# Kernel optimization log

Hardware: AMD Instinct MI355X
Metric: run time of the kernel (lower is better)

The kernel has to match this reference:

```python
import jax, jax.numpy as jnp
import numpy as np

H, DK, DV, DM = 16, 64, 64, 1024
TEMP = float(np.power(DK, 0.5))
EPS = 1e-5


def setup_inputs() -> dict:
    key = jax.random.key(0)
    ks = jax.random.split(key, 12)
    B, LQ, LK = 2, 2048, 2048
    q = jax.random.normal(ks[0], (B, LQ, DM), jnp.float32)
    k = jax.random.normal(ks[1], (B, LK, DM), jnp.float32)
    v = jax.random.normal(ks[2], (B, LK, DM), jnp.float32)
    # projection weights, torch Linear convention: W [out, in], y = x @ W.T + b
    Wq = jax.random.normal(ks[3], (H * DK, DM), jnp.float32) * np.sqrt(2.0 / (DM + DK))
    Wk = jax.random.normal(ks[4], (H * DK, DM), jnp.float32) * np.sqrt(2.0 / (DM + DK))
    Wv = jax.random.normal(ks[5], (H * DV, DM), jnp.float32) * np.sqrt(2.0 / (DM + DV))
    bq = jnp.zeros((H * DK,), jnp.float32)
    bk = jnp.zeros((H * DK,), jnp.float32)
    bv = jnp.zeros((H * DV,), jnp.float32)
    Wfc = jax.random.normal(ks[6], (DM, H * DV), jnp.float32) * np.sqrt(2.0 / (DM + H * DV))
    bfc = jnp.zeros((DM,), jnp.float32)
    gamma = jnp.ones((DM,), jnp.float32)
    beta = jnp.zeros((DM,), jnp.float32)
    return {"q": q, "k": k, "v": v, "Wq": Wq, "bq": bq, "Wk": Wk, "bk": bk,
            "Wv": Wv, "bv": bv, "Wfc": Wfc, "bfc": bfc, "gamma": gamma, "beta": beta}


def reference(q, k, v, Wq, bq, Wk, bk, Wv, bv, Wfc, bfc, gamma, beta):
    B, LQ, _ = q.shape
    LK = k.shape[1]
    residual = q
    qh = (q @ Wq.T + bq).reshape(B, LQ, H, DK)   # [b, lq, h, dk]
    kh = (k @ Wk.T + bk).reshape(B, LK, H, DK)
    vh = (v @ Wv.T + bv).reshape(B, LK, H, DV)
    # scaled dot-product attention (scores laid out [h, b, lq, lk] to match (h*b) bmm)
    scores = jnp.einsum('bqhd,bkhd->hbqk', qh, kh) / TEMP
    attn = jax.nn.softmax(scores, axis=-1)
    ctx = jnp.einsum('hbqk,bkhd->bqhd', attn, vh).reshape(B, LQ, H * DV)
    out = ctx @ Wfc.T + bfc
    x = out + residual
    mean = jnp.mean(x, axis=-1, keepdims=True)
    var = jnp.var(x, axis=-1, keepdims=True)
    y = (x - mean) / jnp.sqrt(var + EPS) * gamma + beta
    attn_flat = attn.reshape(H * B, LQ, LK)
    q_flat = jnp.transpose(qh, (2, 0, 1, 3)).reshape(H * B, LQ, DK)
    return (y, attn_flat, q_flat)
```

## Files before the change

### kernel.cpp

```cpp
#include <hip/hip_runtime.h>

#define SCALE 0.125f

typedef __attribute__((ext_vector_type(8))) __bf16 bf16x8;
typedef __attribute__((ext_vector_type(4))) float f32x4;

__device__ __forceinline__ unsigned short f2bf(float f) {
    union { float f; unsigned u; } v; v.f = f;
    unsigned r = v.u + 0x7FFF + ((v.u >> 16) & 1);
    return (unsigned short)(r >> 16);
}
__device__ __forceinline__ unsigned pack2bf(float a, float b) {
    return (unsigned)f2bf(a) | ((unsigned)f2bf(b) << 16);
}
#define AS1(p) ((const __attribute__((address_space(1))) void*)(p))
#define AS3(p) ((__attribute__((address_space(3))) void*)(p))

__global__ __launch_bounds__(256) void convert_w_kernel(
    const float* __restrict__ Wq, const float* __restrict__ Wk,
    const float* __restrict__ Wv, const float* __restrict__ Wfc,
    unsigned short* __restrict__ wb)
{
    int t = blockIdx.x * 256 + threadIdx.x;
    int i = t * 8;
    int a = i >> 20;
    int off = i & 1048575;
    const float* src = a == 0 ? Wq : a == 1 ? Wk : a == 2 ? Wv : Wfc;
    float4 v0 = *(const float4*)(src + off);
    float4 v1 = *(const float4*)(src + off + 4);
    unsigned short u[8];
    u[0] = f2bf(v0.x); u[1] = f2bf(v0.y); u[2] = f2bf(v0.z); u[3] = f2bf(v0.w);
    u[4] = f2bf(v1.x); u[5] = f2bf(v1.y); u[6] = f2bf(v1.z); u[7] = f2bf(v1.w);
    *(int4*)&wb[i] = *(int4*)u;
}

__global__ __launch_bounds__(256) void qkv_proj_kernel(
    const float* __restrict__ q, const float* __restrict__ k, const float* __restrict__ v,
    const float* __restrict__ Wq, const float* __restrict__ Wk, const float* __restrict__ Wv,
    const float* __restrict__ bq, const float* __restrict__ bk, const float* __restrict__ bv,
    const unsigned short* __restrict__ Wb,
    unsigned short* __restrict__ qh, unsigned short* __restrict__ kh, unsigned short* __restrict__ vh,
    float* __restrict__ qflat)
{
    __shared__ unsigned short lds_a[128 * 40];
    __shared__ unsigned short lds_b[128 * 40];

    const int nb = blockIdx.x;
    const int mb = blockIdx.y;
    const int proj = nb >> 3;
    const int n0 = (nb & 7) * 128;
    const int m0 = mb * 128;

    const float* X    = proj == 0 ? q  : proj == 1 ? k  : v;
    const float* W    = proj == 0 ? Wq : proj == 1 ? Wk : Wv;
    const float* bias = proj == 0 ? bq : proj == 1 ? bk : bv;
    const unsigned short* WB = Wb ? Wb + (size_t)proj * 1048576 : (const unsigned short*)0;
    unsigned short* OUT = proj == 0 ? qh : proj == 1 ? kh : vh;

    const int t = threadIdx.x;
    const int l = t & 63;
    const int w = t >> 6;
    const int wr = w >> 1, wc = w & 1;
    const int li = l & 15, g = l >> 4;

    f32x4 acc[4][4];
    #pragma unroll
    for (int i = 0; i < 4; i++)
        #pragma unroll
        for (int j = 0; j < 4; j++) acc[i][j] = (f32x4){0.f, 0.f, 0.f, 0.f};

    for (int k0 = 0; k0 < 1024; k0 += 32) {
        #pragma unroll
        for (int i = 0; i < 4; i++) {
            int e = i * 1024 + t * 4;
            int r = e >> 5, c = e & 31;
            float4 av = *(const float4*)(X + (size_t)(m0 + r) * 1024 + k0 + c);
            ushort4 ua; ua.x = f2bf(av.x); ua.y = f2bf(av.y); ua.z = f2bf(av.z); ua.w = f2bf(av.w);
            *(ushort4*)&lds_a[r * 40 + c] = ua;
        }
        if (WB) {
            #pragma unroll
            for (int i = 0; i < 2; i++) {
                int e8 = i * 256 + t;
                int r = e8 >> 2, c8 = e8 & 3;
                int4 wv = *(const int4*)(WB + (size_t)(n0 + r) * 1024 + k0 + c8 * 8);
                *(int4*)&lds_b[r * 40 + c8 * 8] = wv;
            }
        } else {
            #pragma unroll
            for (int i = 0; i < 4; i++) {
                int e = i * 1024 + t * 4;
                int r = e >> 5, c = e & 31;
                float4 bw = *(const float4*)(W + (size_t)(n0 + r) * 1024 + k0 + c);
                ushort4 ub; ub.x = f2bf(bw.x); ub.y = f2bf(bw.y); ub.z = f2bf(bw.z); ub.w = f2bf(bw.w);
                *(ushort4*)&lds_b[r * 40 + c] = ub;
            }
        }
        __syncthreads();
        bf16x8 af[4], bfr[4];
        #pragma unroll
        for (int mi = 0; mi < 4; mi++)
            af[mi] = *(bf16x8*)&lds_a[(wr * 64 + mi * 16 + li) * 40 + g * 8];
        #pragma unroll
        for (int ni = 0; ni < 4; ni++)
            bfr[ni] = *(bf16x8*)&lds_b[(wc * 64 + ni * 16 + li) * 40 + g * 8];
        #pragma unroll
        for (int mi = 0; mi < 4; mi++)
            #pragma unroll
            for (int ni = 0; ni < 4; ni++)
                acc[mi][ni] = __builtin_amdgcn_mfma_f32_16x16x32_bf16(af[mi], bfr[ni], acc[mi][ni], 0, 0, 0);
        __syncthreads();
    }

    #pragma unroll
    for (int mi = 0; mi < 4; mi++)
        #pragma unroll
        for (int ni = 0; ni < 4; ni++) {
            int col = n0 + wc * 64 + ni * 16 + li;
            float bl = bias[col];
            #pragma unroll
            for (int j = 0; j < 4; j++) {
                int row = m0 + wr * 64 + mi * 16 + g * 4 + j;
                float val = acc[mi][ni][j] + bl;
                OUT[(size_t)row * 1024 + col] = f2bf(val);
                if (proj == 0) {
                    int hh = col >> 6, dk = col & 63;
                    int bb = row >> 11, lq = row & 2047;
                    __builtin_nontemporal_store(val,
                        qflat + (((size_t)(hh * 2 + bb)) * 2048 + lq) * 64 + dk);
                }
            }
        }
}

__global__ __launch_bounds__(512) void attn_kernel(
    const unsigned short* __restrict__ qh, const unsigned short* __restrict__ kh,
    const unsigned short* __restrict__ vh, float* __restrict__ attn_out,
    unsigned short* __restrict__ ctx)
{
    __shared__ unsigned short lds_kv[64 * 136];
    __shared__ unsigned short lds_p[128 * 128];

    const int qt = blockIdx.x, hb = blockIdx.y;
    const int h = hb >> 1, b_ = hb & 1;
    const int q0 = qt * 128;
    const int t = threadIdx.x, l = t & 63, w = t >> 6;
    const int li = l & 15, g = l >> 4;

    const unsigned short* Qb = qh + (size_t)(b_ * 2048 + q0) * 1024 + h * 64;
    const unsigned short* Kb = kh + (size_t)(b_ * 2048) * 1024 + h * 64;
    const unsigned short* Vb = vh + (size_t)(b_ * 2048) * 1024 + h * 64;
    float* Ab = attn_out + ((size_t)hb * 2048 + q0) * 2048;

    bf16x8 aq[2];
    #pragma unroll
    for (int kk = 0; kk < 2; kk++)
        aq[kk] = *(const bf16x8*)(Qb + (size_t)(w * 16 + li) * 1024 + kk * 32 + g * 8);

#define STAGE_K(KT) do { \
    _Pragma("unroll") \
    for (int c = 0; c < 2; c++) { \
        int r_ = w * 16 + c * 8 + (l >> 3); \
        int c16s = (l & 7) ^ (r_ & 7); \
        const unsigned short* gp = Kb + (size_t)((KT) * 128 + r_) * 1024 + c16s * 8; \
        __builtin_amdgcn_global_load_lds(AS1(gp), AS3(lds_kv + w * 1024 + c * 512), 16, 0, 0); \
    } } while (0)

    float ssum = 0.f;
    for (int kt = 0; kt < 16; kt++) {
        __syncthreads();
        STAGE_K(kt);
        __syncthreads();
        f32x4 s[8];
        #pragma unroll
        for (int ni = 0; ni < 8; ni++) s[ni] = (f32x4){0.f, 0.f, 0.f, 0.f};
        #pragma unroll
        for (int kk = 0; kk < 2; kk++)
            #pragma unroll
            for (int ni = 0; ni < 8; ni++) {
                int row = ni * 16 + li;
                int us_ = (4 * kk + g) ^ (li & 7);
                bf16x8 bk = *(bf16x8*)&lds_kv[row * 64 + us_ * 8];
                s[ni] = __builtin_amdgcn_mfma_f32_16x16x32_bf16(bk, aq[kk], s[ni], 0, 0, 0);
            }
        float ps = 0.f;
        #pragma unroll
        for (int ni = 0; ni < 8; ni++)
            #pragma unroll
            for (int j = 0; j < 4; j++) ps += __expf(s[ni][j] * SCALE);
        ssum += ps;
    }
    ssum += __shfl_xor(ssum, 16, 64);
    ssum += __shfl_xor(ssum, 32, 64);
    const float rl = 1.f / ssum;

    f32x4 cacc[4];
    #pragma unroll
    for (int ni = 0; ni < 4; ni++) cacc[ni] = (f32x4){0.f, 0.f, 0.f, 0.f};

    for (int kt = 0; kt < 16; kt++) {
        __syncthreads();
        STAGE_K(kt);
        __syncthreads();
        f32x4 s[8];
        #pragma unroll
        for (int ni = 0; ni < 8; ni++) s[ni] = (f32x4){0.f, 0.f, 0.f, 0.f};
        #pragma unroll
        for (int kk = 0; kk < 2; kk++)
            #pragma unroll
            for (int ni = 0; ni < 8; ni++) {
                int row = ni * 16 + li;
                int us_ = (4 * kk + g) ^ (li & 7);
                bf16x8 bk = *(bf16x8*)&lds_kv[row * 64 + us_ * 8];
                s[ni] = __builtin_amdgcn_mfma_f32_16x16x32_bf16(bk, aq[kk], s[ni], 0, 0, 0);
            }
        __syncthreads();
        #pragma unroll
        for (int i = 0; i < 2; i++) {
            int e8 = i * 512 + t;
            int lk = e8 >> 3;
            int dg = (e8 & 7) * 8;
            int4 val = *(const int4*)(Vb + (size_t)(kt * 128 + lk) * 1024 + dg);
            unsigned short us[8]; *(int4*)us = val;
            #pragma unroll
            for (int ii = 0; ii < 8; ii++) {
                int d = dg + ii;
                int lks = lk ^ (((d >> 3) & 7) << 3);
                lds_kv[d * 136 + lks] = us[ii];
            }
        }
        #pragma unroll
        for (int ni = 0; ni < 8; ni++) {
            float p0 = __expf(s[ni][0] * SCALE) * rl;
            float p1 = __expf(s[ni][1] * SCALE) * rl;
            float p2 = __expf(s[ni][2] * SCALE) * rl;
            float p3 = __expf(s[ni][3] * SCALE) * rl;
            f32x4 pv4 = (f32x4){p0, p1, p2, p3};
            __builtin_nontemporal_store(pv4,
                (f32x4*)(Ab + (size_t)(w * 16 + li) * 2048 + kt * 128 + ni * 16 + 4 * g));
            int u = 2 * ni + (g >> 1);
            int us_ = u ^ (li & 7);
            int base = (w * 16 + li) * 128 + us_ * 8 + 4 * (g & 1);
            *(unsigned*)&lds_p[base]     = pack2bf(p0, p1);
            *(unsigned*)&lds_p[base + 2] = pack2bf(p2, p3);
        }
        __syncthreads();
        #pragma unroll
        for (int ks = 0; ks < 4; ks++) {
            int up = (4 * ks + g) ^ (li & 7);
            bf16x8 ap = *(bf16x8*)&lds_p[(w * 16 + li) * 128 + up * 8];
            #pragma unroll
            for (int ni = 0; ni < 4; ni++) {
                int d = ni * 16 + li;
                int lkb = (ks * 32 + g * 8) ^ (((d >> 3) & 7) << 3);
                bf16x8 bv2 = *(bf16x8*)&lds_kv[d * 136 + lkb];
                cacc[ni] = __builtin_amdgcn_mfma_f32_16x16x32_bf16(ap, bv2, cacc[ni], 0, 0, 0);
            }
        }
    }
#undef STAGE_K

    #pragma unroll
    for (int ni = 0; ni < 4; ni++)
        #pragma unroll
        for (int j = 0; j < 4; j++) {
            int r = w * 16 + g * 4 + j;
            int d = ni * 16 + li;
            ctx[(size_t)(b_ * 2048 + q0 + r) * 1024 + h * 64 + d] = f2bf(cacc[ni][j]);
        }
}

__global__ __launch_bounds__(256) void fc_kernel(
    const unsigned short* __restrict__ ctx, const float* __restrict__ Wfc,
    const unsigned short* __restrict__ Wfcb,
    const float* __restrict__ bfc, const float* __restrict__ resid,
    float* __restrict__ xout)
{
    __shared__ unsigned short lds_a[128 * 40];
    __shared__ unsigned short lds_b[128 * 40];

    const int n0 = blockIdx.x * 128;
    const int m0 = blockIdx.y * 128;
    const int t = threadIdx.x, l = t & 63, w = t >> 6;
    const int wr = w >> 1, wc = w & 1;
    const int li = l & 15, g = l >> 4;

    f32x4 acc[4][4];
    #pragma unroll
    for (int i = 0; i < 4; i++)
        #pragma unroll
        for (int j = 0; j < 4; j++) acc[i][j] = (f32x4){0.f, 0.f, 0.f, 0.f};

    for (int k0 = 0; k0 < 1024; k0 += 32) {
        #pragma unroll
        for (int i = 0; i < 2; i++) {
            int e = i * 2048 + t * 8;
            int r = e >> 5, c = e & 31;
            int4 val = *(const int4*)(ctx + (size_t)(m0 + r) * 1024 + k0 + c);
            *(int4*)&lds_a[r * 40 + c] = val;
        }
        if (Wfcb) {
            #pragma unroll
            for (int i = 0; i < 2; i++) {
                int e8 = i * 256 + t;
                int r = e8 >> 2, c8 = e8 & 3;
                int4 wv = *(const int4*)(Wfcb + (size_t)(n0 + r) * 1024 + k0 + c8 * 8);
                *(int4*)&lds_b[r * 40 + c8 * 8] = wv;
            }
        } else {
            #pragma unroll
            for (int i = 0; i < 4; i++) {
                int e = i * 1024 + t * 4;
                int r = e >> 5, c = e & 31;
                float4 bw = *(const float4*)(Wfc + (size_t)(n0 + r) * 1024 + k0 + c);
                ushort4 ub; ub.x = f2bf(bw.x); ub.y = f2bf(bw.y); ub.z = f2bf(bw.z); ub.w = f2bf(bw.w);
                *(ushort4*)&lds_b[r * 40 + c] = ub;
            }
        }
        __syncthreads();
        bf16x8 af[4], bfr[4];
        #pragma unroll
        for (int mi = 0; mi < 4; mi++)
            af[mi] = *(bf16x8*)&lds_a[(wr * 64 + mi * 16 + li) * 40 + g * 8];
        #pragma unroll
        for (int ni = 0; ni < 4; ni++)
            bfr[ni] = *(bf16x8*)&lds_b[(wc * 64 + ni * 16 + li) * 40 + g * 8];
        #pragma unroll
        for (int mi = 0; mi < 4; mi++)
            #pragma unroll
            for (int ni = 0; ni < 4; ni++)
                acc[mi][ni] = __builtin_amdgcn_mfma_f32_16x16x32_bf16(af[mi], bfr[ni], acc[mi][ni], 0, 0, 0);
        __syncthreads();
    }

    #pragma unroll
    for (int mi = 0; mi < 4; mi++)
        #pragma unroll
        for (int ni = 0; ni < 4; ni++) {
            int col = n0 + wc * 64 + ni * 16 + li;
            float bl = bfc[col];
            #pragma unroll
            for (int j = 0; j < 4; j++) {
                int row = m0 + wr * 64 + mi * 16 + g * 4 + j;
                float val = acc[mi][ni][j] + bl + resid[(size_t)row * 1024 + col];
                xout[(size_t)row * 1024 + col] = val;
            }
        }
}

__global__ __launch_bounds__(256) void ln_kernel(
    const float* __restrict__ x, const float* __restrict__ gamma,
    const float* __restrict__ beta, float* __restrict__ y)
{
    __shared__ float red[2][4];
    const int row = blockIdx.x;
    const int t = threadIdx.x;
    float4 v = *(const float4*)(x + (size_t)row * 1024 + t * 4);
    float s = v.x + v.y + v.z + v.w;
    float ss = v.x * v.x + v.y * v.y + v.z * v.z + v.w * v.w;
    #pragma unroll
    for (int msk = 1; msk < 64; msk <<= 1) {
        s += __shfl_xor(s, msk, 64);
        ss += __shfl_xor(ss, msk, 64);
    }
    int w = t >> 6, l = t & 63;
    if (l == 0) { red[0][w] = s; red[1][w] = ss; }
    __syncthreads();
    s = red[0][0] + red[0][1] + red[0][2] + red[0][3];
    ss = red[1][0] + red[1][1] + red[1][2] + red[1][3];
    float mean = s * (1.f / 1024.f);
    float var = ss * (1.f / 1024.f) - mean * mean;
    float rstd = rsqrtf(var + 1e-5f);
    float4 g4 = *(const float4*)(gamma + t * 4);
    float4 b4 = *(const float4*)(beta + t * 4);
    float4 o;
    o.x = (v.x - mean) * rstd * g4.x + b4.x;
    o.y = (v.y - mean) * rstd * g4.y + b4.y;
    o.z = (v.z - mean) * rstd * g4.z + b4.z;
    o.w = (v.w - mean) * rstd * g4.w + b4.w;
    *(float4*)(y + (size_t)row * 1024 + t * 4) = o;
}

extern "C" void kernel_launch(void* const* d_in, const int* in_sizes, int n_in,
                              void* d_out, int out_size, void* d_ws, size_t ws_size,
                              hipStream_t stream)
{
    const float* q     = (const float*)d_in[0];
    const float* k     = (const float*)d_in[1];
    const float* v     = (const float*)d_in[2];
    const float* Wq    = (const float*)d_in[3];
    const float* bq    = (const float*)d_in[4];
    const float* Wk    = (const float*)d_in[5];
    const float* bk    = (const float*)d_in[6];
    const float* Wv    = (const float*)d_in[7];
    const float* bv    = (const float*)d_in[8];
    const float* Wfc   = (const float*)d_in[9];
    const float* bfc   = (const float*)d_in[10];
    const float* gamma = (const float*)d_in[11];
    const float* beta  = (const float*)d_in[12];

    float* y     = (float*)d_out;
    float* attn  = (float*)d_out + 4194304;
    float* qflat = (float*)d_out + 4194304 + 134217728;

    char* ws = (char*)d_ws;
    unsigned short* qh  = (unsigned short*)(ws);
    unsigned short* kh  = (unsigned short*)(ws + 8388608ull);
    unsigned short* vh  = (unsigned short*)(ws + 16777216ull);
    unsigned short* ctx = (unsigned short*)(ws + 25165824ull);
    float* x            = (float*)(ws + 33554432ull);
    unsigned short* Wb  = (unsigned short*)(ws + 50331648ull);
    const bool pre = ws_size >= 58720256ull;
    const unsigned short* Wbp = pre ? Wb : (const unsigned short*)0;

    if (pre)
        convert_w_kernel<<<2048, 256, 0, stream>>>(Wq, Wk, Wv, Wfc, Wb);
    qkv_proj_kernel<<<dim3(24, 32), 256, 0, stream>>>(q, k, v, Wq, Wk, Wv, bq, bk, bv,
                                                      Wbp, qh, kh, vh, qflat);
    attn_kernel<<<dim3(16, 32), 512, 0, stream>>>(qh, kh, vh, attn, ctx);
    fc_kernel<<<dim3(8, 32), 256, 0, stream>>>(ctx, Wfc, pre ? Wb + 3145728 : (const unsigned short*)0,
                                               bfc, q, x);
    ln_kernel<<<4096, 256, 0, stream>>>(x, gamma, beta, y);
}
```

Baseline: 318.9 us.

## Pre-convert activations to bf16, async LDS loads, double-buffer K and pre-transpose V

Activations q/k/v are converted to bf16 up front, staged temporarily in the attn output buffer. The QKV and FC GEMMs now use direct global-to-LDS loads with a 64-wide K step and swizzled layout. Attention double-buffers K tiles and reads V from a pre-transposed layout written by the QKV epilogue, which removes the scalar transpose scatter into LDS. LayerNorm runs in place on the output, and the workspace layout and launch bounds change. These changes add an extra conversion pass over the inputs and make correctness depend on the attn buffer being overwritten after use.

Result: faster. 309.9 us (-2.8%).

```diff
diff --git a/kernel.cpp b/kernel.cpp
--- a/kernel.cpp
+++ b/kernel.cpp
@@ -16,34 +16,44 @@
 #define AS1(p) ((const __attribute__((address_space(1))) void*)(p))
 #define AS3(p) ((__attribute__((address_space(3))) void*)(p))
 
-__global__ __launch_bounds__(256) void convert_w_kernel(
+__global__ __launch_bounds__(256) void convert_kernel(
+    const float* __restrict__ q, const float* __restrict__ k, const float* __restrict__ v,
     const float* __restrict__ Wq, const float* __restrict__ Wk,
     const float* __restrict__ Wv, const float* __restrict__ Wfc,
-    unsigned short* __restrict__ wb)
-{
-    int t = blockIdx.x * 256 + threadIdx.x;
-    int i = t * 8;
-    int a = i >> 20;
-    int off = i & 1048575;
-    const float* src = a == 0 ? Wq : a == 1 ? Wk : a == 2 ? Wv : Wfc;
+    unsigned short* __restrict__ xb, unsigned short* __restrict__ wb)
+{
+    size_t i = ((size_t)blockIdx.x * 256 + threadIdx.x) * 8;
+    const float* src;
+    unsigned short* dst;
+    size_t off;
+    if (i < 12582912ull) {
+        int a = (int)(i >> 22);
+        src = a == 0 ? q : a == 1 ? k : v;
+        off = i & 4194303ull;
+        dst = xb + i;
+    } else {
+        size_t wi = i - 12582912ull;
+        int a = (int)(wi >> 20);
+        src = a == 0 ? Wq : a == 1 ? Wk : a == 2 ? Wv : Wfc;
+        off = wi & 1048575ull;
+        dst = wb + wi;
+    }
     float4 v0 = *(const float4*)(src + off);
     float4 v1 = *(const float4*)(src + off + 4);
     unsigned short u[8];
     u[0] = f2bf(v0.x); u[1] = f2bf(v0.y); u[2] = f2bf(v0.z); u[3] = f2bf(v0.w);
     u[4] = f2bf(v1.x); u[5] = f2bf(v1.y); u[6] = f2bf(v1.z); u[7] = f2bf(v1.w);
-    *(int4*)&wb[i] = *(int4*)u;
-}
-
-__global__ __launch_bounds__(256) void qkv_proj_kernel(
-    const float* __restrict__ q, const float* __restrict__ k, const float* __restrict__ v,
-    const float* __restrict__ Wq, const float* __restrict__ Wk, const float* __restrict__ Wv,
+    *(int4*)dst = *(int4*)u;
+}
+
+__global__ __launch_bounds__(256, 3) void qkv_proj_kernel(
+    const unsigned short* __restrict__ xb, const unsigned short* __restrict__ wb,
     const float* __restrict__ bq, const float* __restrict__ bk, const float* __restrict__ bv,
-    const unsigned short* __restrict__ Wb,
-    unsigned short* __restrict__ qh, unsigned short* __restrict__ kh, unsigned short* __restrict__ vh,
-    float* __restrict__ qflat)
-{
-    __shared__ unsigned short lds_a[128 * 40];
-    __shared__ unsigned short lds_b[128 * 40];
+    unsigned short* __restrict__ qh, unsigned short* __restrict__ kh,
+    unsigned short* __restrict__ vht, float* __restrict__ qflat)
+{
+    __shared__ unsigned short lds_a[128 * 64];
+    __shared__ unsigned short lds_b[128 * 64];
 
     const int nb = blockIdx.x;
     const int mb = blockIdx.y;
@@ -51,17 +61,15 @@
     const int n0 = (nb & 7) * 128;
     const int m0 = mb * 128;
 
-    const float* X    = proj == 0 ? q  : proj == 1 ? k  : v;
-    const float* W    = proj == 0 ? Wq : proj == 1 ? Wk : Wv;
+    const unsigned short* A = xb + (size_t)proj * 4194304;
+    const unsigned short* B = wb + (size_t)proj * 1048576;
     const float* bias = proj == 0 ? bq : proj == 1 ? bk : bv;
-    const unsigned short* WB = Wb ? Wb + (size_t)proj * 1048576 : (const unsigned short*)0;
-    unsigned short* OUT = proj == 0 ? qh : proj == 1 ? kh : vh;
-
-    const int t = threadIdx.x;
-    const int l = t & 63;
-    const int w = t >> 6;
+
+    const int t = threadIdx.x, l = t & 63, w = t >> 6;
     const int wr = w >> 1, wc = w & 1;
     const int li = l & 15, g = l >> 4;
+    const int sr = l >> 3;
+    const int us_st = (l & 7) ^ sr;
 
     f32x4 acc[4][4];
     #pragma unroll
@@ -69,76 +77,84 @@
         #pragma unroll
         for (int j = 0; j < 4; j++) acc[i][j] = (f32x4){0.f, 0.f, 0.f, 0.f};
 
-    for (int k0 = 0; k0 < 1024; k0 += 32) {
+    for (int k0 = 0; k0 < 1024; k0 += 64) {
+        __syncthreads();
         #pragma unroll
         for (int i = 0; i < 4; i++) {
-            int e = i * 1024 + t * 4;
-            int r = e >> 5, c = e & 31;
-            float4 av = *(const float4*)(X + (size_t)(m0 + r) * 1024 + k0 + c);
-            ushort4 ua; ua.x = f2bf(av.x); ua.y = f2bf(av.y); ua.z = f2bf(av.z); ua.w = f2bf(av.w);
-            *(ushort4*)&lds_a[r * 40 + c] = ua;
-        }
-        if (WB) {
-            #pragma unroll
-            for (int i = 0; i < 2; i++) {
-                int e8 = i * 256 + t;
-                int r = e8 >> 2, c8 = e8 & 3;
-                int4 wv = *(const int4*)(WB + (size_t)(n0 + r) * 1024 + k0 + c8 * 8);
-                *(int4*)&lds_b[r * 40 + c8 * 8] = wv;
-            }
-        } else {
-            #pragma unroll
-            for (int i = 0; i < 4; i++) {
-                int e = i * 1024 + t * 4;
-                int r = e >> 5, c = e & 31;
-                float4 bw = *(const float4*)(W + (size_t)(n0 + r) * 1024 + k0 + c);
-                ushort4 ub; ub.x = f2bf(bw.x); ub.y = f2bf(bw.y); ub.z = f2bf(bw.z); ub.w = f2bf(bw.w);
-                *(ushort4*)&lds_b[r * 40 + c] = ub;
-            }
-        }
-        __syncthreads();
-        bf16x8 af[4], bfr[4];
+            int r = i * 32 + w * 8 + sr;
+            __builtin_amdgcn_global_load_lds(AS1(A + (size_t)(m0 + r) * 1024 + k0 + us_st * 8),
+                                             AS3(lds_a + (i * 256 + w * 64) * 8), 16, 0, 0);
+            __builtin_amdgcn_global_load_lds(AS1(B + (size_t)(n0 + r) * 1024 + k0 + us_st * 8),
+                                             AS3(lds_b + (i * 256 + w * 64) * 8), 16, 0, 0);
+        }
+        __syncthreads();
+        #pragma unroll
+        for (int kk = 0; kk < 2; kk++) {
+            bf16x8 af[4], bfr[4];
+            int us = (kk * 4 + g) ^ (li & 7);
+            #pragma unroll
+            for (int mi = 0; mi < 4; mi++)
+                af[mi] = *(bf16x8*)&lds_a[(wr * 64 + mi * 16 + li) * 64 + us * 8];
+            #pragma unroll
+            for (int ni = 0; ni < 4; ni++)
+                bfr[ni] = *(bf16x8*)&lds_b[(wc * 64 + ni * 16 + li) * 64 + us * 8];
+            #pragma unroll
+            for (int mi = 0; mi < 4; mi++)
+                #pragma unroll
+                for (int ni = 0; ni < 4; ni++)
+                    acc[mi][ni] = __builtin_amdgcn_mfma_f32_16x16x32_bf16(af[mi], bfr[ni], acc[mi][ni], 0, 0, 0);
+        }
+    }
+
+    if (proj == 2) {
         #pragma unroll
         for (int mi = 0; mi < 4; mi++)
-            af[mi] = *(bf16x8*)&lds_a[(wr * 64 + mi * 16 + li) * 40 + g * 8];
-        #pragma unroll
-        for (int ni = 0; ni < 4; ni++)
-            bfr[ni] = *(bf16x8*)&lds_b[(wc * 64 + ni * 16 + li) * 40 + g * 8];
+            #pragma unroll
+            for (int ni = 0; ni < 4; ni++) {
+                int c = n0 + wc * 64 + ni * 16 + li;
+                float bl = bias[c];
+                int hh = c >> 6, dd = c & 63;
+                int row0 = m0 + wr * 64 + mi * 16 + g * 4;
+                int bb = row0 >> 11, kk2 = row0 & 2047;
+                ushort4 u4;
+                u4.x = f2bf(acc[mi][ni][0] + bl);
+                u4.y = f2bf(acc[mi][ni][1] + bl);
+                u4.z = f2bf(acc[mi][ni][2] + bl);
+                u4.w = f2bf(acc[mi][ni][3] + bl);
+                *(ushort4*)(vht + ((size_t)((bb * 16 + hh) * 64 + dd)) * 2048 + kk2) = u4;
+            }
+    } else {
+        unsigned short* OUT = proj == 0 ? qh : kh;
         #pragma unroll
         for (int mi = 0; mi < 4; mi++)
             #pragma unroll
-            for (int ni = 0; ni < 4; ni++)
-                acc[mi][ni] = __builtin_amdgcn_mfma_f32_16x16x32_bf16(af[mi], bfr[ni], acc[mi][ni], 0, 0, 0);
-        __syncthreads();
-    }
-
-    #pragma unroll
-    for (int mi = 0; mi < 4; mi++)
-        #pragma unroll
-        for (int ni = 0; ni < 4; ni++) {
-            int col = n0 + wc * 64 + ni * 16 + li;
-            float bl = bias[col];
-            #pragma unroll
-            for (int j = 0; j < 4; j++) {
-                int row = m0 + wr * 64 + mi * 16 + g * 4 + j;
-                float val = acc[mi][ni][j] + bl;
-                OUT[(size_t)row * 1024 + col] = f2bf(val);
-                if (proj == 0) {
-                    int hh = col >> 6, dk = col & 63;
-                    int bb = row >> 11, lq = row & 2047;
-                    __builtin_nontemporal_store(val,
-                        qflat + (((size_t)(hh * 2 + bb)) * 2048 + lq) * 64 + dk);
+            for (int ni = 0; ni < 4; ni++) {
+                int c = n0 + wc * 64 + ni * 16 + li;
+                float bl = bias[c];
+                int hh = c >> 6, dd = c & 63;
+                int row0 = m0 + wr * 64 + mi * 16 + g * 4;
+                #pragma unroll
+                for (int j = 0; j < 4; j++) {
+                    int row = row0 + j;
+                    float val = acc[mi][ni][j] + bl;
+                    OUT[(size_t)row * 1024 + c] = f2bf(val);
+                    if (proj == 0) {
+                        int bb = row >> 11, lq = row & 2047;
+                        __builtin_nontemporal_store(val,
+                            qflat + (((size_t)(hh * 2 + bb)) * 2048 + lq) * 64 + dd);
+                    }
                 }
             }
-        }
-}
-
-__global__ __launch_bounds__(512) void attn_kernel(
+    }
+}
+
+__global__ __launch_bounds__(512, 4) void attn_kernel(
     const unsigned short* __restrict__ qh, const unsigned short* __restrict__ kh,
-    const unsigned short* __restrict__ vh, float* __restrict__ attn_out,
+    const unsigned short* __restrict__ vht, float* __restrict__ attn_out,
     unsigned short* __restrict__ ctx)
 {
-    __shared__ unsigned short lds_kv[64 * 136];
+    __shared__ unsigned short lds_k[2][128 * 64];
+    __shared__ unsigned short lds_vt[64 * 128];
     __shared__ unsigned short lds_p[128 * 128];
 
     const int qt = blockIdx.x, hb = blockIdx.y;
@@ -149,7 +165,7 @@
 
     const unsigned short* Qb = qh + (size_t)(b_ * 2048 + q0) * 1024 + h * 64;
     const unsigned short* Kb = kh + (size_t)(b_ * 2048) * 1024 + h * 64;
-    const unsigned short* Vb = vh + (size_t)(b_ * 2048) * 1024 + h * 64;
+    const unsigned short* VTb = vht + (size_t)(b_ * 16 + h) * 131072;
     float* Ab = attn_out + ((size_t)hb * 2048 + q0) * 2048;
 
     bf16x8 aq[2];
@@ -157,38 +173,48 @@
     for (int kk = 0; kk < 2; kk++)
         aq[kk] = *(const bf16x8*)(Qb + (size_t)(w * 16 + li) * 1024 + kk * 32 + g * 8);
 
-#define STAGE_K(KT) do { \
+    const int sr8 = l >> 3;
+    const int us8 = (l & 7) ^ sr8;
+
+#define STAGE_K(KT, BUF) do { \
     _Pragma("unroll") \
     for (int c = 0; c < 2; c++) { \
-        int r_ = w * 16 + c * 8 + (l >> 3); \
-        int c16s = (l & 7) ^ (r_ & 7); \
-        const unsigned short* gp = Kb + (size_t)((KT) * 128 + r_) * 1024 + c16s * 8; \
-        __builtin_amdgcn_global_load_lds(AS1(gp), AS3(lds_kv + w * 1024 + c * 512), 16, 0, 0); \
+        int r_ = w * 16 + c * 8 + sr8; \
+        __builtin_amdgcn_global_load_lds(AS1(Kb + (size_t)((KT) * 128 + r_) * 1024 + us8 * 8), \
+            AS3(lds_k[BUF] + w * 1024 + c * 512), 16, 0, 0); \
     } } while (0)
 
+    const int vd0 = w * 4 + g;
+    const int vd1 = vd0 + 32;
+    const int vslot0 = (li ^ (vd0 & 7)) * 8;
+    const int vslot1 = (li ^ (vd1 & 7)) * 8;
+
     float ssum = 0.f;
+    int cur = 0;
+    STAGE_K(0, 0);
+    __syncthreads();
     for (int kt = 0; kt < 16; kt++) {
-        __syncthreads();
-        STAGE_K(kt);
-        __syncthreads();
+        if (kt < 15) STAGE_K(kt + 1, cur ^ 1);
         f32x4 s[8];
         #pragma unroll
         for (int ni = 0; ni < 8; ni++) s[ni] = (f32x4){0.f, 0.f, 0.f, 0.f};
         #pragma unroll
-        for (int kk = 0; kk < 2; kk++)
+        for (int kk = 0; kk < 2; kk++) {
+            int us = ((kk * 4 + g) ^ (li & 7)) * 8;
             #pragma unroll
             for (int ni = 0; ni < 8; ni++) {
-                int row = ni * 16 + li;
-                int us_ = (4 * kk + g) ^ (li & 7);
-                bf16x8 bk = *(bf16x8*)&lds_kv[row * 64 + us_ * 8];
+                bf16x8 bk = *(bf16x8*)&lds_k[cur][(ni * 16 + li) * 64 + us];
                 s[ni] = __builtin_amdgcn_mfma_f32_16x16x32_bf16(bk, aq[kk], s[ni], 0, 0, 0);
             }
+        }
         float ps = 0.f;
         #pragma unroll
         for (int ni = 0; ni < 8; ni++)
             #pragma unroll
             for (int j = 0; j < 4; j++) ps += __expf(s[ni][j] * SCALE);
         ssum += ps;
+        __syncthreads();
+        cur ^= 1;
     }
     ssum += __shfl_xor(ssum, 16, 64);
     ssum += __shfl_xor(ssum, 32, 64);
@@ -198,35 +224,30 @@
     #pragma unroll
     for (int ni = 0; ni < 4; ni++) cacc[ni] = (f32x4){0.f, 0.f, 0.f, 0.f};
 
+    STAGE_K(0, cur);
+    int4 vt0 = *(const int4*)(VTb + (size_t)vd0 * 2048 + li * 8);
+    int4 vt1 = *(const int4*)(VTb + (size_t)vd1 * 2048 + li * 8);
+    __syncthreads();
+    *(int4*)&lds_vt[vd0 * 128 + vslot0] = vt0;
+    *(int4*)&lds_vt[vd1 * 128 + vslot1] = vt1;
+    __syncthreads();
+
     for (int kt = 0; kt < 16; kt++) {
-        __syncthreads();
-        STAGE_K(kt);
-        __syncthreads();
+        if (kt < 15) {
+            STAGE_K(kt + 1, cur ^ 1);
+            vt0 = *(const int4*)(VTb + (size_t)vd0 * 2048 + (kt + 1) * 128 + li * 8);
+            vt1 = *(const int4*)(VTb + (size_t)vd1 * 2048 + (kt + 1) * 128 + li * 8);
+        }
         f32x4 s[8];
         #pragma unroll
         for (int ni = 0; ni < 8; ni++) s[ni] = (f32x4){0.f, 0.f, 0.f, 0.f};
         #pragma unroll
-        for (int kk = 0; kk < 2; kk++)
+        for (int kk = 0; kk < 2; kk++) {
+            int us = ((kk * 4 + g) ^ (li & 7)) * 8;
             #pragma unroll
             for (int ni = 0; ni < 8; ni++) {
-                int row = ni * 16 + li;
-                int us_ = (4 * kk + g) ^ (li & 7);
-                bf16x8 bk = *(bf16x8*)&lds_kv[row * 64 + us_ * 8];
+                bf16x8 bk = *(bf16x8*)&lds_k[cur][(ni * 16 + li) * 64 + us];
                 s[ni] = __builtin_amdgcn_mfma_f32_16x16x32_bf16(bk, aq[kk], s[ni], 0, 0, 0);
-            }
-        __syncthreads();
-        #pragma unroll
-        for (int i = 0; i < 2; i++) {
-            int e8 = i * 512 + t;
-            int lk = e8 >> 3;
-            int dg = (e8 & 7) * 8;
-            int4 val = *(const int4*)(Vb + (size_t)(kt * 128 + lk) * 1024 + dg);
-            unsigned short us[8]; *(int4*)us = val;
-            #pragma unroll
-            for (int ii = 0; ii < 8; ii++) {
-                int d = dg + ii;
-                int lks = lk ^ (((d >> 3) & 7) << 3);
-                lds_kv[d * 136 + lks] = us[ii];
             }
         }
         #pragma unroll
@@ -238,25 +259,28 @@
             f32x4 pv4 = (f32x4){p0, p1, p2, p3};
             __builtin_nontemporal_store(pv4,
                 (f32x4*)(Ab + (size_t)(w * 16 + li) * 2048 + kt * 128 + ni * 16 + 4 * g));
-            int u = 2 * ni + (g >> 1);
-            int us_ = u ^ (li & 7);
+            int us_ = (2 * ni + (g >> 1)) ^ (li & 7);
             int base = (w * 16 + li) * 128 + us_ * 8 + 4 * (g & 1);
             *(unsigned*)&lds_p[base]     = pack2bf(p0, p1);
             *(unsigned*)&lds_p[base + 2] = pack2bf(p2, p3);
         }
-        __syncthreads();
         #pragma unroll
         for (int ks = 0; ks < 4; ks++) {
-            int up = (4 * ks + g) ^ (li & 7);
-            bf16x8 ap = *(bf16x8*)&lds_p[(w * 16 + li) * 128 + up * 8];
+            int us = ((ks * 4 + g) ^ (li & 7)) * 8;
+            bf16x8 ap = *(bf16x8*)&lds_p[(w * 16 + li) * 128 + us];
             #pragma unroll
             for (int ni = 0; ni < 4; ni++) {
-                int d = ni * 16 + li;
-                int lkb = (ks * 32 + g * 8) ^ (((d >> 3) & 7) << 3);
-                bf16x8 bv2 = *(bf16x8*)&lds_kv[d * 136 + lkb];
+                bf16x8 bv2 = *(bf16x8*)&lds_vt[(ni * 16 + li) * 128 + us];
                 cacc[ni] = __builtin_amdgcn_mfma_f32_16x16x32_bf16(ap, bv2, cacc[ni], 0, 0, 0);
             }
         }
+        __syncthreads();
+        if (kt < 15) {
+            *(int4*)&lds_vt[vd0 * 128 + vslot0] = vt0;
+            *(int4*)&lds_vt[vd1 * 128 + vslot1] = vt1;
+        }
+        __syncthreads();
+        cur ^= 1;
     }
 #undef STAGE_K
 
@@ -270,20 +294,21 @@
         }
 }
 
-__global__ __launch_bounds__(256) void fc_kernel(
-    const unsigned short* __restrict__ ctx, const float* __restrict__ Wfc,
-    const unsigned short* __restrict__ Wfcb,
+__global__ __launch_bounds__(256, 3) void fc_kernel(
+    const unsigned short* __restrict__ ctx, const unsigned short* __restrict__ wfcb,
     const float* __restrict__ bfc, const float* __restrict__ resid,
     float* __restrict__ xout)
 {
-    __shared__ unsigned short lds_a[128 * 40];
-    __shared__ unsigned short lds_b[128 * 40];
+    __shared__ unsigned short lds_a[128 * 64];
+    __shared__ unsigned short lds_b[128 * 64];
 
     const int n0 = blockIdx.x * 128;
     const int m0 = blockIdx.y * 128;
     const int t = threadIdx.x, l = t & 63, w = t >> 6;
     const int wr = w >> 1, wc = w & 1;
     const int li = l & 15, g = l >> 4;
+    const int sr = l >> 3;
+    const int us_st = (l & 7) ^ sr;
 
     f32x4 acc[4][4];
     #pragma unroll
@@ -291,46 +316,33 @@
         #pragma unroll
         for (int j = 0; j < 4; j++) acc[i][j] = (f32x4){0.f, 0.f, 0.f, 0.f};
 
-    for (int k0 = 0; k0 < 1024; k0 += 32) {
-        #pragma unroll
-        for (int i = 0; i < 2; i++) {
-            int e = i * 2048 + t * 8;
-            int r = e >> 5, c = e & 31;
-            int4 val = *(const int4*)(ctx + (size_t)(m0 + r) * 1024 + k0 + c);
-            *(int4*)&lds_a[r * 40 + c] = val;
-        }
-        if (Wfcb) {
-            #pragma unroll
-            for (int i = 0; i < 2; i++) {
-                int e8 = i * 256 + t;
-                int r = e8 >> 2, c8 = e8 & 3;
-                int4 wv = *(const int4*)(Wfcb + (size_t)(n0 + r) * 1024 + k0 + c8 * 8);
-                *(int4*)&lds_b[r * 40 + c8 * 8] = wv;
-            }
-        } else {
-            #pragma unroll
-            for (int i = 0; i < 4; i++) {
-                int e = i * 1024 + t * 4;
-                int r = e >> 5, c = e & 31;
-                float4 bw = *(const float4*)(Wfc + (size_t)(n0 + r) * 1024 + k0 + c);
-                ushort4 ub; ub.x = f2bf(bw.x); ub.y = f2bf(bw.y); ub.z = f2bf(bw.z); ub.w = f2bf(bw.w);
-                *(ushort4*)&lds_b[r * 40 + c] = ub;
-            }
-        }
-        __syncthreads();
-        bf16x8 af[4], bfr[4];
-        #pragma unroll
-        for (int mi = 0; mi < 4; mi++)
-            af[mi] = *(bf16x8*)&lds_a[(wr * 64 + mi * 16 + li) * 40 + g * 8];
-        #pragma unroll
-        for (int ni = 0; ni < 4; ni++)
-            bfr[ni] = *(bf16x8*)&lds_b[(wc * 64 + ni * 16 + li) * 40 + g * 8];
-        #pragma unroll
-        for (int mi = 0; mi < 4; mi++)
+    for (int k0 = 0; k0 < 1024; k0 += 64) {
+        __syncthreads();
+        #pragma unroll
+        for (int i = 0; i < 4; i++) {
+            int r = i * 32 + w * 8 + sr;
+            __builtin_amdgcn_global_load_lds(AS1(ctx + (size_t)(m0 + r) * 1024 + k0 + us_st * 8),
+                                             AS3(lds_a + (i * 256 + w * 64) * 8), 16, 0, 0);
+            __builtin_amdgcn_global_load_lds(AS1(wfcb + (size_t)(n0 + r) * 1024 + k0 + us_st * 8),
+                                             AS3(lds_b + (i * 256 + w * 64) * 8), 16, 0, 0);
+        }
+        __syncthreads();
+        #pragma unroll
+        for (int kk = 0; kk < 2; kk++) {
+            bf16x8 af[4], bfr[4];
+            int us = (kk * 4 + g) ^ (li & 7);
+            #pragma unroll
+            for (int mi = 0; mi < 4; mi++)
+                af[mi] = *(bf16x8*)&lds_a[(wr * 64 + mi * 16 + li) * 64 + us * 8];
             #pragma unroll
             for (int ni = 0; ni < 4; ni++)
-                acc[mi][ni] = __builtin_amdgcn_mfma_f32_16x16x32_bf16(af[mi], bfr[ni], acc[mi][ni], 0, 0, 0);
-        __syncthreads();
+                bfr[ni] = *(bf16x8*)&lds_b[(wc * 64 + ni * 16 + li) * 64 + us * 8];
+            #pragma unroll
+            for (int mi = 0; mi < 4; mi++)
+                #pragma unroll
+                for (int ni = 0; ni < 4; ni++)
+                    acc[mi][ni] = __builtin_amdgcn_mfma_f32_16x16x32_bf16(af[mi], bfr[ni], acc[mi][ni], 0, 0, 0);
+        }
     }
 
     #pragma unroll
@@ -349,8 +361,8 @@
 }
 
 __global__ __launch_bounds__(256) void ln_kernel(
-    const float* __restrict__ x, const float* __restrict__ gamma,
-    const float* __restrict__ beta, float* __restrict__ y)
+    float* __restrict__ x, const float* __restrict__ gamma,
+    const float* __restrict__ beta)
 {
     __shared__ float red[2][4];
     const int row = blockIdx.x;
@@ -378,7 +390,7 @@
     o.y = (v.y - mean) * rstd * g4.y + b4.y;
     o.z = (v.z - mean) * rstd * g4.z + b4.z;
     o.w = (v.w - mean) * rstd * g4.w + b4.w;
-    *(float4*)(y + (size_t)row * 1024 + t * 4) = o;
+    *(float4*)(x + (size_t)row * 1024 + t * 4) = o;
 }
 
 extern "C" void kernel_launch(void* const* d_in, const int* in_sizes, int n_in,
@@ -403,22 +415,18 @@
     float* attn  = (float*)d_out + 4194304;
     float* qflat = (float*)d_out + 4194304 + 134217728;
 
+    unsigned short* xb = (unsigned short*)attn;
+
     char* ws = (char*)d_ws;
     unsigned short* qh  = (unsigned short*)(ws);
     unsigned short* kh  = (unsigned short*)(ws + 8388608ull);
-    unsigned short* vh  = (unsigned short*)(ws + 16777216ull);
+    unsigned short* vht = (unsigned short*)(ws + 16777216ull);
     unsigned short* ctx = (unsigned short*)(ws + 25165824ull);
-    float* x            = (float*)(ws + 33554432ull);
-    unsigned short* Wb  = (unsigned short*)(ws + 50331648ull);
-    const bool pre = ws_size >= 58720256ull;
-    const unsigned short* Wbp = pre ? Wb : (const unsigned short*)0;
-
-    if (pre)
-        convert_w_kernel<<<2048, 256, 0, stream>>>(Wq, Wk, Wv, Wfc, Wb);
-    qkv_proj_kernel<<<dim3(24, 32), 256, 0, stream>>>(q, k, v, Wq, Wk, Wv, bq, bk, bv,
-                                                      Wbp, qh, kh, vh, qflat);
-    attn_kernel<<<dim3(16, 32), 512, 0, stream>>>(qh, kh, vh, attn, ctx);
-    fc_kernel<<<dim3(8, 32), 256, 0, stream>>>(ctx, Wfc, pre ? Wb + 3145728 : (const unsigned short*)0,
-                                               bfc, q, x);
-    ln_kernel<<<4096, 256, 0, stream>>>(x, gamma, beta, y);
-}
+    unsigned short* wb  = (unsigned short*)(ws + 33554432ull);
+
+    convert_kernel<<<8192, 256, 0, stream>>>(q, k, v, Wq, Wk, Wv, Wfc, xb, wb);
+    qkv_proj_kernel<<<dim3(24, 32), 256, 0, stream>>>(xb, wb, bq, bk, bv, qh, kh, vht, qflat);
+    attn_kernel<<<dim3(16, 32), 512, 0, stream>>>(qh, kh, vht, attn, ctx);
+    fc_kernel<<<dim3(8, 32), 256, 0, stream>>>(ctx, wb + 3145728, bfc, q, y);
+    ln_kernel<<<4096, 256, 0, stream>>>(y, gamma, beta);
+}
```
